# Performance work log

Hardware: AMD Instinct MI355X
Metric: run time of the kernel (lower is better)

Reference implementation:

```python
import jax, jax.numpy as jnp
import numpy as np

N, E, G = 10000, 160000, 64          # nodes, edges, graphs in batch
X_IN, HID, EDIM, H = 128, 128, 32, 4  # feature dims, edge dim, heads
NEG_SLOPE = 0.2


def setup_inputs() -> dict:
    key = jax.random.key(0)
    ks = jax.random.split(key, 24)
    def p(k, shape):
        return jax.random.normal(k, shape, jnp.float32) * 0.1
    inp = {
        "x": jax.random.normal(ks[0], (N, X_IN), jnp.float32),
        "edge_index": jax.random.randint(ks[1], (2, E), 0, N),
        "edge_attr": jax.random.normal(ks[2], (E, EDIM), jnp.float32),
        "batch": jnp.sort(jax.random.randint(ks[3], (N,), 0, G)),
    }
    dims = [(X_IN, HID), (HID, 2 * HID), (2 * HID, HID)]
    i = 4
    for l, (cin, cout) in enumerate(dims, 1):
        inp[f"W{l}"] = p(ks[i], (cin, H * cout)); i += 1   # node lin (bias-free, PyG default)
        inp[f"We{l}"] = p(ks[i], (EDIM, H * cout)); i += 1  # edge lin (bias=False in PyG)
        inp[f"as{l}"] = p(ks[i], (H, cout)); i += 1         # att_src
        inp[f"ad{l}"] = p(ks[i], (H, cout)); i += 1         # att_dst
        inp[f"ae{l}"] = p(ks[i], (H, cout)); i += 1         # att_edge
        inp[f"b{l}"] = jnp.zeros((cout,), jnp.float32); i += 1
    return inp


def _add_self_loops(src, dst, eattr, n):
    # PyG GATConv default: add_self_loops=True, fill_value='mean' ->
    # self-loop edge_attr = scatter-mean of incoming edge_attr per node.
    deg = jax.ops.segment_sum(jnp.ones_like(dst, jnp.float32), dst, num_segments=n)
    mean_e = jax.ops.segment_sum(eattr, dst, num_segments=n) / jnp.maximum(deg, 1.0)[:, None]
    loop = jnp.arange(n)
    return (jnp.concatenate([src, loop]), jnp.concatenate([dst, loop]),
            jnp.concatenate([eattr, mean_e], axis=0))


def _segment_softmax(logits, seg, n):
    # logits: [E2, H], softmax over edges grouped by destination node
    m = jax.ops.segment_max(logits, seg, num_segments=n)
    m = jnp.where(jnp.isfinite(m), m, 0.0)
    ex = jnp.exp(logits - m[seg])
    s = jax.ops.segment_sum(ex, seg, num_segments=n)
    return ex / (s[seg] + 1e-16)


def _gat_layer(x, src, dst, eattr, W, We, a_s, a_d, a_e, b, n):
    heads, cout = a_s.shape
    xs = (x @ W).reshape(n, heads, cout)            # [N,H,C]
    ee = (eattr @ We).reshape(-1, heads, cout)      # [E2,H,C]
    al_src = jnp.sum(xs * a_s, axis=-1)             # [N,H]
    al_dst = jnp.sum(xs * a_d, axis=-1)             # [N,H]
    al_edge = jnp.sum(ee * a_e, axis=-1)            # [E2,H]
    logits = jax.nn.leaky_relu(al_src[src] + al_dst[dst] + al_edge, NEG_SLOPE)
    alpha = _segment_softmax(logits, dst, n)        # [E2,H]
    out = jax.ops.segment_sum(alpha[:, :, None] * xs[src], dst, num_segments=n)
    return out.mean(axis=1) + b                     # concat=False -> mean over heads


def reference(x, edge_index, edge_attr, batch,
              W1, We1, as1, ad1, ae1, b1,
              W2, We2, as2, ad2, ae2, b2,
              W3, We3, as3, ad3, ae3, b3):
    src, dst = edge_index[0], edge_index[1]
    src2, dst2, e2 = _add_self_loops(src, dst, edge_attr, N)
    h = jax.nn.elu(_gat_layer(x, src2, dst2, e2, W1, We1, as1, ad1, ae1, b1, N))
    h = jax.nn.elu(_gat_layer(h, src2, dst2, e2, W2, We2, as2, ad2, ae2, b2, N))
    h = jax.nn.elu(_gat_layer(h, src2, dst2, e2, W3, We3, as3, ad3, ae3, b3, N))
    cnt = jax.ops.segment_sum(jnp.ones((N,), jnp.float32), batch, num_segments=G)
    return jax.ops.segment_sum(h, batch, num_segments=G) / jnp.maximum(cnt, 1.0)[:, None]
```

## Files before the change

kernel.cpp:

```cpp
#include <hip/hip_runtime.h>

#define NN 10000
#define NE 160000
#define NE2 (NE + NN)
#define NG 64
#define EDIM 32

typedef _Float16 f16;
typedef __attribute__((ext_vector_type(2))) _Float16 f16x2;
typedef __attribute__((ext_vector_type(4))) _Float16 f16x4;
typedef __attribute__((ext_vector_type(8))) _Float16 f16x8;
typedef __attribute__((ext_vector_type(4))) float f32x4;
typedef __attribute__((ext_vector_type(8))) unsigned short u16x8;

__device__ __forceinline__ float lrelu(float x) { return fmaxf(x, 0.2f * x); }
__device__ __forceinline__ float elu1(float x) { return x > 0.f ? x : __expf(x) - 1.f; }


template <int CIN, int C>
__device__ __forceinline__ void wprep_body(int b, int tid,
                                           const float* __restrict__ W,
                                           const float* __restrict__ We,
                                           const float* __restrict__ as_,
                                           const float* __restrict__ ad_,
                                           const float* __restrict__ ae_,
                                           f16* __restrict__ Bt,
                                           float* __restrict__ asd,
                                           float* __restrict__ Wf,
                                           float (*t)[33]) {
    constexpr int K4 = 4 * CIN;
    constexpr int KT = CIN / 32, CT = C / 32;
    constexpr int TB = 4 * KT * CT;
    constexpr int FB = CIN / 64;
    if (b < TB) {
        int h = b / (KT * CT);
        int rem = b % (KT * CT);
        int k0 = (rem / CT) * 32, c0 = (rem % CT) * 32;
        int i = tid >> 5, j = tid & 31;
#pragma unroll
        for (int it = 0; it < 4; ++it)
            t[i + it * 8][j] = W[(size_t)(k0 + i + it * 8) * (4 * C) + h * C + c0 + j];
        __syncthreads();
#pragma unroll
        for (int it = 0; it < 4; ++it) {
            int jj = (tid >> 5) + it * 8, ii = tid & 31;
            Bt[(size_t)(c0 + jj) * K4 + h * CIN + k0 + ii] = (f16)t[ii][jj];
        }
    } else if (b < TB + FB) {
        int k = (b - TB) * 64 + (tid >> 2), h = tid & 3;
        const float4* wr = (const float4*)(W + (size_t)k * (4 * C) + h * C);
        const float4* a4 = (const float4*)(as_ + h * C);
        const float4* d4 = (const float4*)(ad_ + h * C);
        float s = 0.f, d = 0.f;
        for (int c = 0; c < C / 4; ++c) {
            float4 w = wr[c], av = a4[c], dv = d4[c];
            s += w.x * av.x + w.y * av.y + w.z * av.z + w.w * av.w;
            d += w.x * dv.x + w.y * dv.y + w.z * dv.z + w.w * dv.w;
        }
        asd[h * CIN + k] = s;
        asd[4 * CIN + h * CIN + k] = d;
    } else if (tid < 128) {
        int dd = tid >> 2, h = tid & 3;
        const float4* wr = (const float4*)(We + (size_t)dd * (4 * C) + h * C);
        const float4* a4 = (const float4*)(ae_ + h * C);
        float s = 0.f;
        for (int c = 0; c < C / 4; ++c) {
            float4 w = wr[c], av = a4[c];
            s += w.x * av.x + w.y * av.y + w.z * av.z + w.w * av.w;
        }
        Wf[dd * 4 + h] = s;
    }
}


__global__ __launch_bounds__(256) void k_init(
    const float* W1, const float* We1, const float* as1, const float* ad1, const float* ae1,
    f16* Bt1, float* asd1, float* Wf1,
    const float* W2, const float* We2, const float* as2, const float* ad2, const float* ae2,
    f16* Bt2, float* asd2, float* Wf2,
    const float* W3, const float* We3, const float* as3, const float* ad3, const float* ae3,
    f16* Bt3, float* asd3, float* Wf3,
    const int* ei, int* deg, const float* x, f16* x16,
    const int* batch, float* invc) {
    __shared__ float t[32][33];
    int b = blockIdx.x, tid = threadIdx.x;
    if (b < 67) {
        wprep_body<128, 128>(b, tid, W1, We1, as1, ad1, ae1, Bt1, asd1, Wf1, t);
    } else if (b < 198) {
        wprep_body<128, 256>(b - 67, tid, W2, We2, as2, ad2, ae2, Bt2, asd2, Wf2, t);
    } else if (b < 331) {
        wprep_body<256, 128>(b - 198, tid, W3, We3, as3, ad3, ae3, Bt3, asd3, Wf3, t);
    } else if (b < 956) {
        int e = (b - 331) * 256 + tid;
        atomicAdd(&deg[ei[NE + e]], 1);
    } else if (b < 2206) {
        int i = (b - 956) * 256 + tid;
        float4 v = ((const float4*)x)[i];
        f16x4 o;
        o[0] = (f16)v.x; o[1] = (f16)v.y; o[2] = (f16)v.z; o[3] = (f16)v.w;
        *(f16x4*)(x16 + i * 4) = o;
    } else if (tid < NG) {
        int g = tid;
        int lo = 0, hi = NN;
        while (lo < hi) { int mid = (lo + hi) >> 1; if (batch[mid] < g) lo = mid + 1; else hi = mid; }
        int start = lo;
        lo = start; hi = NN;
        while (lo < hi) { int mid = (lo + hi) >> 1; if (batch[mid] < g + 1) lo = mid + 1; else hi = mid; }
        invc[g] = 1.f / fmaxf((float)(lo - start), 1.f);
    }
}


__global__ __launch_bounds__(1024) void k_scan2(const int* __restrict__ deg,
                                                int* __restrict__ row_ptr,
                                                int* __restrict__ cursor) {
    int tid = threadIdx.x;
    int vals[10];
    int run = 0;
#pragma unroll
    for (int i = 0; i < 10; ++i) {
        int n = tid * 10 + i;
        int v = (n < NN) ? (deg[n] + 1) : 0;
        run += v;
        vals[i] = run;
    }
    int total = run;
    int lane = tid & 63, wid = tid >> 6;
    int sc = total;
#pragma unroll
    for (int off = 1; off < 64; off <<= 1) {
        int t = __shfl_up(sc, off);
        if (lane >= off) sc += t;
    }
    __shared__ int wsum[16];
    if (lane == 63) wsum[wid] = sc;
    __syncthreads();
    if (tid == 0) {
        int a = 0;
#pragma unroll
        for (int w = 0; w < 16; ++w) { int t = wsum[w]; wsum[w] = a; a += t; }
    }
    __syncthreads();
    int excl = sc - total + wsum[wid];
#pragma unroll
    for (int i = 0; i < 10; ++i) {
        int n = tid * 10 + i;
        if (n < NN) {
            int prev = i ? vals[i - 1] : 0;
            row_ptr[n + 1] = excl + vals[i];
            cursor[n] = excl + prev;
        }
    }
    if (tid == 0) row_ptr[0] = 0;
}


__global__ __launch_bounds__(256) void k_fill_e4(const int* __restrict__ ei,
                                                 int* __restrict__ cursor,
                                                 int* __restrict__ src_sorted,
                                                 int* __restrict__ selfpos,
                                                 const float* __restrict__ eattr,
                                                 const float* __restrict__ Wf1,
                                                 const float* __restrict__ Wf2,
                                                 const float* __restrict__ Wf3,
                                                 float* __restrict__ e4all,
                                                 const f16* __restrict__ x16,
                                                 const float* __restrict__ asd1,
                                                 float* __restrict__ als1,
                                                 float* __restrict__ ald1) {
    __shared__ float smem[1024];
    int b = blockIdx.x, tid = threadIdx.x;
    if (b < 665) {
        for (int i = tid; i < 384; i += 256)
            smem[i] = (i < 128) ? Wf1[i] : (i < 256) ? Wf2[i - 128] : Wf3[i - 256];
        __syncthreads();
        int e = b * 256 + tid;
        if (e >= NE2) return;
        if (e < NE) {
            int s = ei[e], d = ei[NE + e];
            int p = atomicAdd(&cursor[d], 1);
            src_sorted[p] = s;
            float4 v[8];
            const float4* er = (const float4*)(eattr + (size_t)e * EDIM);
#pragma unroll
            for (int i = 0; i < 8; ++i) v[i] = er[i];
#pragma unroll
            for (int l = 0; l < 3; ++l) {
                float a0 = 0.f, a1 = 0.f, a2 = 0.f, a3 = 0.f;
#pragma unroll
                for (int d4 = 0; d4 < 8; ++d4) {
                    const float* w = &smem[l * 128 + d4 * 16];
                    a0 += v[d4].x * w[0] + v[d4].y * w[4] + v[d4].z * w[8]  + v[d4].w * w[12];
                    a1 += v[d4].x * w[1] + v[d4].y * w[5] + v[d4].z * w[9]  + v[d4].w * w[13];
                    a2 += v[d4].x * w[2] + v[d4].y * w[6] + v[d4].z * w[10] + v[d4].w * w[14];
                    a3 += v[d4].x * w[3] + v[d4].y * w[7] + v[d4].z * w[11] + v[d4].w * w[15];
                }
                ((float4*)e4all)[(size_t)l * NE2 + p] = make_float4(a0, a1, a2, a3);
            }
        } else {
            int n = e - NE;
            int p = atomicAdd(&cursor[n], 1);
            src_sorted[p] = n;
            selfpos[n] = p;
        }
    } else {
        float* sA = smem;
        float* sD = smem + 512;
        for (int i = tid; i < 512; i += 256) { sA[i] = asd1[i]; sD[i] = asd1[512 + i]; }
        __syncthreads();
        int wid = tid >> 6, lane = tid & 63;
        int node = (b - 665) * 4 + wid;
        int h = lane >> 4, c16 = lane & 15;
        const f16* xr = x16 + (size_t)node * 128 + c16 * 8;
        f16x8 v = *(const f16x8*)xr;
        float s = 0.f, d = 0.f;
#pragma unroll
        for (int i = 0; i < 8; ++i) {
            float f = (float)v[i];
            s += f * sA[h * 128 + c16 * 8 + i];
            d += f * sD[h * 128 + c16 * 8 + i];
        }
#pragma unroll
        for (int off = 1; off < 16; off <<= 1) { s += __shfl_xor(s, off); d += __shfl_xor(d, off); }
        if (c16 == 0) { als1[node * 4 + h] = s; ald1[node * 4 + h] = d; }
    }
}


template <int CIN>
__global__ __launch_bounds__(256) void k_alnode2(const f16* __restrict__ xp,
                                                 const float* __restrict__ asd,
                                                 float* __restrict__ als,
                                                 float* __restrict__ ald) {
    __shared__ float sA[4 * CIN], sD[4 * CIN];
    for (int i = threadIdx.x; i < 4 * CIN; i += 256) { sA[i] = asd[i]; sD[i] = asd[4 * CIN + i]; }
    __syncthreads();
    int wid = threadIdx.x >> 6, lane = threadIdx.x & 63;
    int node = blockIdx.x * 4 + wid;
    int h = lane >> 4, c16 = lane & 15;
    constexpr int KC = CIN / 16;
    const f16* xr = xp + (size_t)node * CIN + c16 * KC;
    float s = 0.f, d = 0.f;
#pragma unroll
    for (int p = 0; p < KC / 8; ++p) {
        f16x8 v = *(const f16x8*)(xr + p * 8);
        const float* wa = &sA[h * CIN + c16 * KC + p * 8];
        const float* wd = &sD[h * CIN + c16 * KC + p * 8];
#pragma unroll
        for (int i = 0; i < 8; ++i) {
            float f = (float)v[i];
            s += f * wa[i];
            d += f * wd[i];
        }
    }
#pragma unroll
    for (int off = 1; off < 16; off <<= 1) { s += __shfl_xor(s, off); d += __shfl_xor(d, off); }
    if (c16 == 0) { als[node * 4 + h] = s; ald[node * 4 + h] = d; }
}


template <int CIN, int WPN>
__global__ __launch_bounds__(256) void k_agg2(const int* __restrict__ row_ptr,
                                              const int* __restrict__ src_sorted,
                                              const int* __restrict__ selfpos,
                                              const float* __restrict__ e4,
                                              const float* __restrict__ als,
                                              const float* __restrict__ ald,
                                              const f16* __restrict__ xp,
                                              f16* __restrict__ aggcat) {
    constexpr int CHUNK = CIN / WPN;
    constexpr int EPL = CHUNK / 64;
    constexpr int NPB = 4 / WPN;
    int wid = threadIdx.x >> 6, lane = threadIdx.x & 63;
    int node = blockIdx.x * NPB + wid / WPN;
    int half = wid % WPN;
    int beg = row_ptr[node], end = row_ptr[node + 1];
    int sp = selfpos[node];
    float4 ad4 = ((const float4*)ald)[node];
    const float4* e44 = (const float4*)e4;
    const float4* als4 = (const float4*)als;
    float s0 = 0.f, s1 = 0.f, s2 = 0.f, s3 = 0.f;
    float es0 = 0.f, es1 = 0.f, es2 = 0.f, es3 = 0.f;
    float a0[EPL] = {}, a1[EPL] = {}, a2[EPL] = {}, a3[EPL] = {};
    const f16* xbase = xp + half * CHUNK + lane * EPL;
#pragma unroll 4
    for (int j = beg; j < end; ++j) {
        if (j == sp) continue;
        int src = src_sorted[j];
        float4 ev = e44[j];
        es0 += ev.x; es1 += ev.y; es2 += ev.z; es3 += ev.w;
        float4 av = als4[src];
        float e0 = __expf(lrelu(ev.x + av.x + ad4.x));
        float e1 = __expf(lrelu(ev.y + av.y + ad4.y));
        float e2 = __expf(lrelu(ev.z + av.z + ad4.z));
        float e3 = __expf(lrelu(ev.w + av.w + ad4.w));
        s0 += e0; s1 += e1; s2 += e2; s3 += e3;
        const f16* xr = xbase + (size_t)src * CIN;
        f16x2 v = *(const f16x2*)xr;
        float f0 = (float)v[0], f1 = (float)v[1];
        a0[0] += e0 * f0; a0[1] += e0 * f1;
        a1[0] += e1 * f0; a1[1] += e1 * f1;
        a2[0] += e2 * f0; a2[1] += e2 * f1;
        a3[0] += e3 * f0; a3[1] += e3 * f1;
    }
    {
        float inv = 1.f / fmaxf((float)(end - beg - 1), 1.f);
        float4 sv = als4[node];
        float e0 = __expf(lrelu(es0 * inv + sv.x + ad4.x));
        float e1 = __expf(lrelu(es1 * inv + sv.y + ad4.y));
        float e2 = __expf(lrelu(es2 * inv + sv.z + ad4.z));
        float e3 = __expf(lrelu(es3 * inv + sv.w + ad4.w));
        s0 += e0; s1 += e1; s2 += e2; s3 += e3;
        const f16* xr = xbase + (size_t)node * CIN;
        f16x2 v = *(const f16x2*)xr;
        float f0 = (float)v[0], f1 = (float)v[1];
        a0[0] += e0 * f0; a0[1] += e0 * f1;
        a1[0] += e1 * f0; a1[1] += e1 * f1;
        a2[0] += e2 * f0; a2[1] += e2 * f1;
        a3[0] += e3 * f0; a3[1] += e3 * f1;
    }
    float i0 = 1.f / (s0 + 1e-16f), i1 = 1.f / (s1 + 1e-16f);
    float i2 = 1.f / (s2 + 1e-16f), i3 = 1.f / (s3 + 1e-16f);
    f16* ob = aggcat + (size_t)node * 4 * CIN + half * CHUNK + lane * EPL;
    f16x2 o;
    o[0] = (f16)(a0[0] * i0); o[1] = (f16)(a0[1] * i0); *(f16x2*)(ob + 0 * CIN) = o;
    o[0] = (f16)(a1[0] * i1); o[1] = (f16)(a1[1] * i1); *(f16x2*)(ob + 1 * CIN) = o;
    o[0] = (f16)(a2[0] * i2); o[1] = (f16)(a2[1] * i2); *(f16x2*)(ob + 2 * CIN) = o;
    o[0] = (f16)(a3[0] * i3); o[1] = (f16)(a3[1] * i3); *(f16x2*)(ob + 3 * CIN) = o;
}


template <int K4, int C, bool POOL>
__global__ __launch_bounds__(256) void k_gemm2(const f16* __restrict__ A,
                                               const f16* __restrict__ Bt,
                                               const float* __restrict__ bias,
                                               f16* __restrict__ hout,
                                               const int* __restrict__ batch,
                                               const float* __restrict__ invc,
                                               float* __restrict__ out) {
    constexpr int NS = K4 / 32;
    __shared__ f16 Als[2][32 * 32];
    __shared__ f16 Bls[2][64 * 32];
    __shared__ float pacc[4][64];
    int bm = blockIdx.x * 32, bn = blockIdx.y * 64;
    int tid = threadIdx.x;
    int wid = tid >> 6, lane = tid & 63;
    int mq = wid >> 1, nq = wid & 1;
    int fr = lane & 15, kc = lane >> 4;

    if (POOL) pacc[tid >> 6][tid & 63] = 0.f;

    int ar = tid >> 2, ac = tid & 3;
    const f16* Ap = A + (size_t)(bm + (ar & 31)) * K4 + ac * 8;
    const f16* Bp = Bt + (size_t)(bn + ar) * K4 + ac * 8;
    bool aok = (tid < 128) && (bm + ar < NN);
    int wA = (ar & 31) * 32 + ((ac ^ (ar & 3)) * 8);
    int wB = ar * 32 + ((ac ^ (ar & 3)) * 8);
    int kx = (kc ^ (fr & 3)) * 8;
    int rA = (mq * 16 + fr) * 32 + kx;
    int rB0 = (nq * 32 + fr) * 32 + kx;
    int rB1 = rB0 + 16 * 32;

    f32x4 acc0 = (f32x4){0.f, 0.f, 0.f, 0.f};
    f32x4 acc1 = (f32x4){0.f, 0.f, 0.f, 0.f};

    u16x8 va = (u16x8)0, vb;
    if (aok) va = *(const u16x8*)Ap;
    vb = *(const u16x8*)Bp;
    if (tid < 128) *(u16x8*)&Als[0][wA] = va;
    *(u16x8*)&Bls[0][wB] = vb;
    __syncthreads();

#pragma unroll
    for (int s = 0; s < NS; ++s) {
        int cur = s & 1;
        if (s + 1 < NS) {
            va = (u16x8)0;
            if (aok) va = *(const u16x8*)(Ap + (s + 1) * 32);
            vb = *(const u16x8*)(Bp + (s + 1) * 32);
        }
        f16x8 af  = *(const f16x8*)&Als[cur][rA];
        f16x8 bf0 = *(const f16x8*)&Bls[cur][rB0];
        f16x8 bf1 = *(const f16x8*)&Bls[cur][rB1];
        acc0 = __builtin_amdgcn_mfma_f32_16x16x32_f16(af, bf0, acc0, 0, 0, 0);
        acc1 = __builtin_amdgcn_mfma_f32_16x16x32_f16(af, bf1, acc1, 0, 0, 0);
        if (s + 1 < NS) {
            if (tid < 128) *(u16x8*)&Als[cur ^ 1][wA] = va;
            *(u16x8*)&Bls[cur ^ 1][wB] = vb;
        }
        __syncthreads();
    }

    int cr = kc * 4, cc = fr;
    int lc0 = nq * 32 + cc, lc1 = lc0 + 16;
    int col0 = bn + lc0, col1 = bn + lc1;
    float b0 = bias[col0], b1 = bias[col1];
    int g0 = POOL ? batch[bm] : 0;
#pragma unroll
    for (int r = 0; r < 4; ++r) {
        int row = bm + mq * 16 + cr + r;
        if (row >= NN) continue;
        float v0 = elu1(0.25f * acc0[r] + b0);
        float v1 = elu1(0.25f * acc1[r] + b1);
        if (POOL) {
            int g = batch[row];
            float ic = invc[g];
            int wi = g - g0;
            if (wi < 4) {
                atomicAdd(&pacc[wi][lc0], v0 * ic);
                atomicAdd(&pacc[wi][lc1], v1 * ic);
            } else {
                atomicAdd(&out[(size_t)g * C + col0], v0 * ic);
                atomicAdd(&out[(size_t)g * C + col1], v1 * ic);
            }
        } else {
            f16* cp = hout + (size_t)row * C + col0;
            cp[0] = (f16)v0;
            cp[16] = (f16)v1;
        }
    }
    if (POOL) {
        __syncthreads();
        int wi = tid >> 6, c = tid & 63;
        float val = pacc[wi][c];
        int g = g0 + wi;
        if (val != 0.f && g < NG)
            atomicAdd(&out[(size_t)g * C + bn + c], val);
    }
}


struct Ws {
    f16 *x16, *hA, *hB, *aggcat, *Wt1, *Wt2, *Wt3;
    float *als1, *ald1, *als2, *ald2, *als3, *ald3;
    float *e4all, *asd1, *asd2, *asd3, *Wf1, *Wf2, *Wf3, *invc;
    int *deg, *row_ptr, *cursor, *src_sorted, *selfpos;
};

static void carve(void* base, Ws& w) {
    char* p = (char*)base;
    size_t off = 0;
    auto take = [&](size_t bytes) {
        off = (off + 255) & ~(size_t)255;
        void* r = p + off;
        off += bytes;
        return r;
    };
    w.x16        = (f16*)take((size_t)NN * 128 * 2);
    w.hA         = (f16*)take((size_t)NN * 128 * 2);
    w.hB         = (f16*)take((size_t)NN * 256 * 2);
    w.aggcat     = (f16*)take((size_t)NN * 1024 * 2);
    w.Wt1        = (f16*)take((size_t)512 * 128 * 2);
    w.Wt2        = (f16*)take((size_t)512 * 256 * 2);
    w.Wt3        = (f16*)take((size_t)1024 * 128 * 2);
    w.als1       = (float*)take((size_t)NN * 4 * 4);
    w.ald1       = (float*)take((size_t)NN * 4 * 4);
    w.als2       = (float*)take((size_t)NN * 4 * 4);
    w.ald2       = (float*)take((size_t)NN * 4 * 4);
    w.als3       = (float*)take((size_t)NN * 4 * 4);
    w.ald3       = (float*)take((size_t)NN * 4 * 4);
    w.e4all      = (float*)take((size_t)3 * NE2 * 4 * 4);
    w.asd1       = (float*)take(2 * 4 * 128 * 4);
    w.asd2       = (float*)take(2 * 4 * 128 * 4);
    w.asd3       = (float*)take(2 * 4 * 256 * 4);
    w.Wf1        = (float*)take(128 * 4);
    w.Wf2        = (float*)take(128 * 4);
    w.Wf3        = (float*)take(128 * 4);
    w.invc       = (float*)take(NG * 4);
    w.deg        = (int*)take((size_t)NN * 4);
    w.row_ptr    = (int*)take((size_t)(NN + 1) * 4);
    w.cursor     = (int*)take((size_t)NN * 4);
    w.src_sorted = (int*)take((size_t)NE2 * 4);
    w.selfpos    = (int*)take((size_t)NN * 4);
}

extern "C" void kernel_launch(void* const* d_in, const int* in_sizes, int n_in,
                              void* d_out, int out_size, void* d_ws, size_t ws_size,
                              hipStream_t stream) {
    const float* x     = (const float*)d_in[0];
    const int*   ei    = (const int*)d_in[1];
    const float* eattr = (const float*)d_in[2];
    const int*   batch = (const int*)d_in[3];
    const float* W[3]  = {(const float*)d_in[4],  (const float*)d_in[10], (const float*)d_in[16]};
    const float* We[3] = {(const float*)d_in[5],  (const float*)d_in[11], (const float*)d_in[17]};
    const float* as_[3]= {(const float*)d_in[6],  (const float*)d_in[12], (const float*)d_in[18]};
    const float* ad_[3]= {(const float*)d_in[7],  (const float*)d_in[13], (const float*)d_in[19]};
    const float* ae_[3]= {(const float*)d_in[8],  (const float*)d_in[14], (const float*)d_in[20]};
    const float* b_[3] = {(const float*)d_in[9],  (const float*)d_in[15], (const float*)d_in[21]};
    float* out = (float*)d_out;

    Ws w;
    carve(d_ws, w);

    hipMemsetAsync(w.deg, 0, (size_t)NN * 4, stream);
    hipMemsetAsync(out, 0, (size_t)NG * 128 * 4, stream);

    k_init<<<2207, 256, 0, stream>>>(
        W[0], We[0], as_[0], ad_[0], ae_[0], w.Wt1, w.asd1, w.Wf1,
        W[1], We[1], as_[1], ad_[1], ae_[1], w.Wt2, w.asd2, w.Wf2,
        W[2], We[2], as_[2], ad_[2], ae_[2], w.Wt3, w.asd3, w.Wf3,
        ei, w.deg, x, w.x16, batch, w.invc);

    k_scan2<<<1, 1024, 0, stream>>>(w.deg, w.row_ptr, w.cursor);

    k_fill_e4<<<3165, 256, 0, stream>>>(ei, w.cursor, w.src_sorted, w.selfpos, eattr,
                                        w.Wf1, w.Wf2, w.Wf3, w.e4all,
                                        w.x16, w.asd1, w.als1, w.ald1);

    const float* e4_1 = w.e4all;
    const float* e4_2 = w.e4all + (size_t)NE2 * 4;
    const float* e4_3 = w.e4all + (size_t)2 * NE2 * 4;

    k_agg2<128, 1><<<NN / 4, 256, 0, stream>>>(w.row_ptr, w.src_sorted, w.selfpos, e4_1,
                                               w.als1, w.ald1, w.x16, w.aggcat);
    k_gemm2<512, 128, false><<<dim3(313, 2), 256, 0, stream>>>(w.aggcat, w.Wt1, b_[0],
                                                               w.hA, nullptr, nullptr, nullptr);
    k_alnode2<128><<<NN / 4, 256, 0, stream>>>(w.hA, w.asd2, w.als2, w.ald2);
    k_agg2<128, 1><<<NN / 4, 256, 0, stream>>>(w.row_ptr, w.src_sorted, w.selfpos, e4_2,
                                               w.als2, w.ald2, w.hA, w.aggcat);
    k_gemm2<512, 256, false><<<dim3(313, 4), 256, 0, stream>>>(w.aggcat, w.Wt2, b_[1],
                                                               w.hB, nullptr, nullptr, nullptr);
    k_alnode2<256><<<NN / 4, 256, 0, stream>>>(w.hB, w.asd3, w.als3, w.ald3);
    k_agg2<256, 2><<<NN / 2, 256, 0, stream>>>(w.row_ptr, w.src_sorted, w.selfpos, e4_3,
                                               w.als3, w.ald3, w.hB, w.aggcat);
    k_gemm2<1024, 128, true><<<dim3(313, 2), 256, 0, stream>>>(w.aggcat, w.Wt3, b_[2],
                                                               nullptr, batch, w.invc, out);
}
```

Baseline: 316.6 us.

## Precompute per-edge attention exponentials and split aggregation edges across wave pairs

Adds a per-edge kernel that computes exp(leaky_relu(edge+src+dst logits)) into a buffer, using a new dst_sorted array, and a kernel that fills in each node's self-loop edge feature mean once up front. The aggregation kernel then reads these precomputed weights and splits each node's edges between two waves, combining their partial sums through shared memory. This takes the exp work and the self-loop special case out of the serial per-node loop and doubles wave parallelism per node. The cost is extra launches, an extra edge-sized buffer round trip through memory, and a block-wide sync in aggregation.

```diff
diff --git a/kernel.cpp b/kernel.cpp
--- a/kernel.cpp
+++ b/kernel.cpp
@@ -158,6 +158,7 @@
 __global__ __launch_bounds__(256) void k_fill_e4(const int* __restrict__ ei,
                                                  int* __restrict__ cursor,
                                                  int* __restrict__ src_sorted,
+                                                 int* __restrict__ dst_sorted,
                                                  int* __restrict__ selfpos,
                                                  const float* __restrict__ eattr,
                                                  const float* __restrict__ Wf1,
@@ -180,6 +181,7 @@
             int s = ei[e], d = ei[NE + e];
             int p = atomicAdd(&cursor[d], 1);
             src_sorted[p] = s;
+            dst_sorted[p] = d;
             float4 v[8];
             const float4* er = (const float4*)(eattr + (size_t)e * EDIM);
 #pragma unroll
@@ -201,6 +203,7 @@
             int n = e - NE;
             int p = atomicAdd(&cursor[n], 1);
             src_sorted[p] = n;
+            dst_sorted[p] = n;
             selfpos[n] = p;
         }
     } else {
@@ -224,6 +227,24 @@
         for (int off = 1; off < 16; off <<= 1) { s += __shfl_xor(s, off); d += __shfl_xor(d, off); }
         if (c16 == 0) { als1[node * 4 + h] = s; ald1[node * 4 + h] = d; }
     }
+}
+
+
+__global__ __launch_bounds__(256) void k_e4self(const int* __restrict__ row_ptr,
+                                                const int* __restrict__ selfpos,
+                                                float* __restrict__ e4all) {
+    int t = blockIdx.x * 256 + threadIdx.x;
+    int node = t >> 4, sub = t & 15;
+    if (sub >= 12) return;
+    int l = sub >> 2, c = sub & 3;
+    int beg = row_ptr[node], end = row_ptr[node + 1];
+    int sp = selfpos[node];
+    const float* base = e4all + (size_t)l * NE2 * 4 + c;
+    float s = 0.f;
+    for (int j = beg; j < end; ++j)
+        if (j != sp) s += base[(size_t)j * 4];
+    float inv = 1.f / fmaxf((float)(end - beg - 1), 1.f);
+    e4all[(size_t)l * NE2 * 4 + (size_t)sp * 4 + c] = s * inv;
 }
 
 
@@ -259,74 +280,83 @@
 }
 
 
-template <int CIN, int WPN>
-__global__ __launch_bounds__(256) void k_agg2(const int* __restrict__ row_ptr,
+__global__ __launch_bounds__(256) void k_t(const float* __restrict__ e4,
+                                           const int* __restrict__ src_sorted,
+                                           const int* __restrict__ dst_sorted,
+                                           const float* __restrict__ als,
+                                           const float* __restrict__ ald,
+                                           float* __restrict__ tbuf) {
+    int j = blockIdx.x * 256 + threadIdx.x;
+    if (j >= NE2) return;
+    float4 ev = ((const float4*)e4)[j];
+    int src = src_sorted[j], dst = dst_sorted[j];
+    float4 sv = ((const float4*)als)[src];
+    float4 dv = ((const float4*)ald)[dst];
+    float4 t;
+    t.x = __expf(lrelu(ev.x + sv.x + dv.x));
+    t.y = __expf(lrelu(ev.y + sv.y + dv.y));
+    t.z = __expf(lrelu(ev.z + sv.z + dv.z));
+    t.w = __expf(lrelu(ev.w + sv.w + dv.w));
+    ((float4*)tbuf)[j] = t;
+}
+
+
+template <int CIN, int CSPLIT>
+__global__ __launch_bounds__(256) void k_agg3(const int* __restrict__ row_ptr,
                                               const int* __restrict__ src_sorted,
-                                              const int* __restrict__ selfpos,
-                                              const float* __restrict__ e4,
-                                              const float* __restrict__ als,
-                                              const float* __restrict__ ald,
+                                              const float* __restrict__ tbuf,
                                               const f16* __restrict__ xp,
                                               f16* __restrict__ aggcat) {
-    constexpr int CHUNK = CIN / WPN;
+    constexpr int CHUNK = CIN / CSPLIT;
     constexpr int EPL = CHUNK / 64;
+    constexpr int WPN = 2 * CSPLIT;
     constexpr int NPB = 4 / WPN;
     int wid = threadIdx.x >> 6, lane = threadIdx.x & 63;
     int node = blockIdx.x * NPB + wid / WPN;
-    int half = wid % WPN;
+    int sub = wid % WPN;
+    int ch = sub >> 1;
+    int ep = sub & 1;
+    int pair = wid >> 1;
     int beg = row_ptr[node], end = row_ptr[node + 1];
-    int sp = selfpos[node];
-    float4 ad4 = ((const float4*)ald)[node];
-    const float4* e44 = (const float4*)e4;
-    const float4* als4 = (const float4*)als;
+    const float4* t4 = (const float4*)tbuf;
     float s0 = 0.f, s1 = 0.f, s2 = 0.f, s3 = 0.f;
-    float es0 = 0.f, es1 = 0.f, es2 = 0.f, es3 = 0.f;
     float a0[EPL] = {}, a1[EPL] = {}, a2[EPL] = {}, a3[EPL] = {};
-    const f16* xbase = xp + half * CHUNK + lane * EPL;
+    const f16* xbase = xp + ch * CHUNK + lane * EPL;
 #pragma unroll 4
-    for (int j = beg; j < end; ++j) {
-        if (j == sp) continue;
+    for (int j = beg + ep; j < end; j += 2) {
+        float4 t = t4[j];
         int src = src_sorted[j];
-        float4 ev = e44[j];
-        es0 += ev.x; es1 += ev.y; es2 += ev.z; es3 += ev.w;
-        float4 av = als4[src];
-        float e0 = __expf(lrelu(ev.x + av.x + ad4.x));
-        float e1 = __expf(lrelu(ev.y + av.y + ad4.y));
-        float e2 = __expf(lrelu(ev.z + av.z + ad4.z));
-        float e3 = __expf(lrelu(ev.w + av.w + ad4.w));
-        s0 += e0; s1 += e1; s2 += e2; s3 += e3;
-        const f16* xr = xbase + (size_t)src * CIN;
-        f16x2 v = *(const f16x2*)xr;
+        s0 += t.x; s1 += t.y; s2 += t.z; s3 += t.w;
+        f16x2 v = *(const f16x2*)(xbase + (size_t)src * CIN);
         float f0 = (float)v[0], f1 = (float)v[1];
-        a0[0] += e0 * f0; a0[1] += e0 * f1;
-        a1[0] += e1 * f0; a1[1] += e1 * f1;
-        a2[0] += e2 * f0; a2[1] += e2 * f1;
-        a3[0] += e3 * f0; a3[1] += e3 * f1;
-    }
-    {
-        float inv = 1.f / fmaxf((float)(end - beg - 1), 1.f);
-        float4 sv = als4[node];
-        float e0 = __expf(lrelu(es0 * inv + sv.x + ad4.x));
-        float e1 = __expf(lrelu(es1 * inv + sv.y + ad4.y));
-        float e2 = __expf(lrelu(es2 * inv + sv.z + ad4.z));
-        float e3 = __expf(lrelu(es3 * inv + sv.w + ad4.w));
-        s0 += e0; s1 += e1; s2 += e2; s3 += e3;
-        const f16* xr = xbase + (size_t)node * CIN;
-        f16x2 v = *(const f16x2*)xr;
-        float f0 = (float)v[0], f1 = (float)v[1];
-        a0[0] += e0 * f0; a0[1] += e0 * f1;
-        a1[0] += e1 * f0; a1[1] += e1 * f1;
-        a2[0] += e2 * f0; a2[1] += e2 * f1;
-        a3[0] += e3 * f0; a3[1] += e3 * f1;
-    }
-    float i0 = 1.f / (s0 + 1e-16f), i1 = 1.f / (s1 + 1e-16f);
-    float i2 = 1.f / (s2 + 1e-16f), i3 = 1.f / (s3 + 1e-16f);
-    f16* ob = aggcat + (size_t)node * 4 * CIN + half * CHUNK + lane * EPL;
-    f16x2 o;
-    o[0] = (f16)(a0[0] * i0); o[1] = (f16)(a0[1] * i0); *(f16x2*)(ob + 0 * CIN) = o;
-    o[0] = (f16)(a1[0] * i1); o[1] = (f16)(a1[1] * i1); *(f16x2*)(ob + 1 * CIN) = o;
-    o[0] = (f16)(a2[0] * i2); o[1] = (f16)(a2[1] * i2); *(f16x2*)(ob + 2 * CIN) = o;
-    o[0] = (f16)(a3[0] * i3); o[1] = (f16)(a3[1] * i3); *(f16x2*)(ob + 3 * CIN) = o;
+        a0[0] += t.x * f0; a0[1] += t.x * f1;
+        a1[0] += t.y * f0; a1[1] += t.y * f1;
+        a2[0] += t.z * f0; a2[1] += t.z * f1;
+        a3[0] += t.w * f0; a3[1] += t.w * f1;
+    }
+    __shared__ float lacc[2][64][8];
+    __shared__ float ls[2][4];
+    if (ep == 0) {
+        float* p = &lacc[pair][lane][0];
+        p[0] = a0[0]; p[1] = a0[1]; p[2] = a1[0]; p[3] = a1[1];
+        p[4] = a2[0]; p[5] = a2[1]; p[6] = a3[0]; p[7] = a3[1];
+        if (lane == 0) { ls[pair][0] = s0; ls[pair][1] = s1; ls[pair][2] = s2; ls[pair][3] = s3; }
+    }
+    __syncthreads();
+    if (ep == 1) {
+        const float* p = &lacc[pair][lane][0];
+        a0[0] += p[0]; a0[1] += p[1]; a1[0] += p[2]; a1[1] += p[3];
+        a2[0] += p[4]; a2[1] += p[5]; a3[0] += p[6]; a3[1] += p[7];
+        s0 += ls[pair][0]; s1 += ls[pair][1]; s2 += ls[pair][2]; s3 += ls[pair][3];
+        float i0 = 1.f / (s0 + 1e-16f), i1 = 1.f / (s1 + 1e-16f);
+        float i2 = 1.f / (s2 + 1e-16f), i3 = 1.f / (s3 + 1e-16f);
+        f16* ob = aggcat + (size_t)node * 4 * CIN + ch * CHUNK + lane * EPL;
+        f16x2 o;
+        o[0] = (f16)(a0[0] * i0); o[1] = (f16)(a0[1] * i0); *(f16x2*)(ob + 0 * CIN) = o;
+        o[0] = (f16)(a1[0] * i1); o[1] = (f16)(a1[1] * i1); *(f16x2*)(ob + 1 * CIN) = o;
+        o[0] = (f16)(a2[0] * i2); o[1] = (f16)(a2[1] * i2); *(f16x2*)(ob + 2 * CIN) = o;
+        o[0] = (f16)(a3[0] * i3); o[1] = (f16)(a3[1] * i3); *(f16x2*)(ob + 3 * CIN) = o;
+    }
 }
 
 
@@ -433,8 +463,8 @@
 struct Ws {
     f16 *x16, *hA, *hB, *aggcat, *Wt1, *Wt2, *Wt3;
     float *als1, *ald1, *als2, *ald2, *als3, *ald3;
-    float *e4all, *asd1, *asd2, *asd3, *Wf1, *Wf2, *Wf3, *invc;
-    int *deg, *row_ptr, *cursor, *src_sorted, *selfpos;
+    float *e4all, *tbuf, *asd1, *asd2, *asd3, *Wf1, *Wf2, *Wf3, *invc;
+    int *deg, *row_ptr, *cursor, *src_sorted, *dst_sorted, *selfpos;
 };
 
 static void carve(void* base, Ws& w) {
@@ -460,6 +490,7 @@
     w.als3       = (float*)take((size_t)NN * 4 * 4);
     w.ald3       = (float*)take((size_t)NN * 4 * 4);
     w.e4all      = (float*)take((size_t)3 * NE2 * 4 * 4);
+    w.tbuf       = (float*)take((size_t)NE2 * 4 * 4);
     w.asd1       = (float*)take(2 * 4 * 128 * 4);
     w.asd2       = (float*)take(2 * 4 * 128 * 4);
     w.asd3       = (float*)take(2 * 4 * 256 * 4);
@@ -471,6 +502,7 @@
     w.row_ptr    = (int*)take((size_t)(NN + 1) * 4);
     w.cursor     = (int*)take((size_t)NN * 4);
     w.src_sorted = (int*)take((size_t)NE2 * 4);
+    w.dst_sorted = (int*)take((size_t)NE2 * 4);
     w.selfpos    = (int*)take((size_t)NN * 4);
 }
 
@@ -503,26 +535,30 @@
 
     k_scan2<<<1, 1024, 0, stream>>>(w.deg, w.row_ptr, w.cursor);
 
-    k_fill_e4<<<3165, 256, 0, stream>>>(ei, w.cursor, w.src_sorted, w.selfpos, eattr,
-                                        w.Wf1, w.Wf2, w.Wf3, w.e4all,
+    k_fill_e4<<<3165, 256, 0, stream>>>(ei, w.cursor, w.src_sorted, w.dst_sorted,
+                                        w.selfpos, eattr, w.Wf1, w.Wf2, w.Wf3, w.e4all,
                                         w.x16, w.asd1, w.als1, w.ald1);
+    k_e4self<<<625, 256, 0, stream>>>(w.row_ptr, w.selfpos, w.e4all);
 
     const float* e4_1 = w.e4all;
     const float* e4_2 = w.e4all + (size_t)NE2 * 4;
     const float* e4_3 = w.e4all + (size_t)2 * NE2 * 4;
 
-    k_agg2<128, 1><<<NN / 4, 256, 0, stream>>>(w.row_ptr, w.src_sorted, w.selfpos, e4_1,
-                                               w.als1, w.ald1, w.x16, w.aggcat);
+    k_t<<<665, 256, 0, stream>>>(e4_1, w.src_sorted, w.dst_sorted, w.als1, w.ald1, w.tbuf);
+    k_agg3<128, 1><<<NN / 2, 256, 0, stream>>>(w.row_ptr, w.src_sorted, w.tbuf,
+                                               w.x16, w.aggcat);
     k_gemm2<512, 128, false><<<dim3(313, 2), 256, 0, stream>>>(w.aggcat, w.Wt1, b_[0],
                                                                w.hA, nullptr, nullptr, nullptr);
     k_alnode2<128><<<NN / 4, 256, 0, stream>>>(w.hA, w.asd2, w.als2, w.ald2);
-    k_agg2<128, 1><<<NN / 4, 256, 0, stream>>>(w.row_ptr, w.src_sorted, w.selfpos, e4_2,
-                                               w.als2, w.ald2, w.hA, w.aggcat);
+    k_t<<<665, 256, 0, stream>>>(e4_2, w.src_sorted, w.dst_sorted, w.als2, w.ald2, w.tbuf);
+    k_agg3<128, 1><<<NN / 2, 256, 0, stream>>>(w.row_ptr, w.src_sorted, w.tbuf,
+                                               w.hA, w.aggcat);
     k_gemm2<512, 256, false><<<dim3(313, 4), 256, 0, stream>>>(w.aggcat, w.Wt2, b_[1],
                                                                w.hB, nullptr, nullptr, nullptr);
     k_alnode2<256><<<NN / 4, 256, 0, stream>>>(w.hB, w.asd3, w.als3, w.ald3);
-    k_agg2<256, 2><<<NN / 2, 256, 0, stream>>>(w.row_ptr, w.src_sorted, w.selfpos, e4_3,
-                                               w.als3, w.ald3, w.hB, w.aggcat);
+    k_t<<<665, 256, 0, stream>>>(e4_3, w.src_sorted, w.dst_sorted, w.als3, w.ald3, w.tbuf);
+    k_agg3<256, 2><<<NN, 256, 0, stream>>>(w.row_ptr, w.src_sorted, w.tbuf,
+                                           w.hB, w.aggcat);
     k_gemm2<1024, 128, true><<<dim3(313, 2), 256, 0, stream>>>(w.aggcat, w.Wt3, b_[2],
                                                                nullptr, batch, w.invc, out);
 }
```

New measurement: 288.3 us. -8.9%, faster.

## Precompute edge attention weights in shared memory and split edges across two waves

Applied to the files above, without the earlier changes.

The aggregation kernel now has the whole block compute each edge's exp-logit once into shared memory, including the self-loop mean edge term via shared atomics, instead of every wave recomputing it. Each node's edge list is then split between two waves that process alternating edges and combine their partial sums through shared memory. This doubles wave-level parallelism per node and cuts redundant exp work and redundant per-edge loads. The cost is extra barriers, shared atomics, and a slow fallback path for nodes with more than 128 edges.

```diff
diff --git a/kernel.cpp b/kernel.cpp
--- a/kernel.cpp
+++ b/kernel.cpp
@@ -259,8 +259,8 @@
 }
 
 
-template <int CIN, int WPN>
-__global__ __launch_bounds__(256) void k_agg2(const int* __restrict__ row_ptr,
+template <int CIN, int CSPLIT>
+__global__ __launch_bounds__(256) void k_agg4(const int* __restrict__ row_ptr,
                                               const int* __restrict__ src_sorted,
                                               const int* __restrict__ selfpos,
                                               const float* __restrict__ e4,
@@ -268,65 +268,164 @@
                                               const float* __restrict__ ald,
                                               const f16* __restrict__ xp,
                                               f16* __restrict__ aggcat) {
-    constexpr int CHUNK = CIN / WPN;
+    constexpr int CHUNK = CIN / CSPLIT;
     constexpr int EPL = CHUNK / 64;
+    constexpr int WPN = 2 * CSPLIT;
     constexpr int NPB = 4 / WPN;
-    int wid = threadIdx.x >> 6, lane = threadIdx.x & 63;
-    int node = blockIdx.x * NPB + wid / WPN;
-    int half = wid % WPN;
+    constexpr int CAP = 128;
+
+    __shared__ float te4[NPB * CAP * 4];
+    __shared__ float lacc[2][64][8];
+    __shared__ float ls[2][4];
+    __shared__ float s4[NPB][4];
+    __shared__ int ovf;
+
+    int tid = threadIdx.x;
+    int wid = tid >> 6, lane = tid & 63;
+    int node0 = blockIdx.x * NPB;
+
+    if (tid < NPB * 4) s4[tid >> 2][tid & 3] = 0.f;
+    if (tid == 0) ovf = 0;
+    __syncthreads();
+
+    int tn = (NPB == 2) ? (tid >> 7) : 0;
+    int ts = (NPB == 2) ? (tid & 127) : tid;
+    int tnode = node0 + tn;
+    int tbeg = row_ptr[tnode];
+    int tcnt = row_ptr[tnode + 1] - tbeg;
+    int tsp = selfpos[tnode];
+    if (ts == 0 && tcnt > CAP) ovf = 1;
+    if (ts < CAP && ts < tcnt) {
+        int j = tbeg + ts;
+        float4 ev = ((const float4*)e4)[j];
+        ((float4*)te4)[tn * CAP + ts] = ev;
+        if (j != tsp) {
+            atomicAdd(&s4[tn][0], ev.x);
+            atomicAdd(&s4[tn][1], ev.y);
+            atomicAdd(&s4[tn][2], ev.z);
+            atomicAdd(&s4[tn][3], ev.w);
+        }
+    }
+    __syncthreads();
+
+    if (!ovf && ts < CAP && ts < tcnt) {
+        int j = tbeg + ts;
+        float4 ev = ((float4*)te4)[tn * CAP + ts];
+        float4 sv;
+        if (j == tsp) {
+            float inv = 1.f / fmaxf((float)(tcnt - 1), 1.f);
+            ev.x = s4[tn][0] * inv; ev.y = s4[tn][1] * inv;
+            ev.z = s4[tn][2] * inv; ev.w = s4[tn][3] * inv;
+            sv = ((const float4*)als)[tnode];
+        } else {
+            sv = ((const float4*)als)[src_sorted[j]];
+        }
+        float4 dv = ((const float4*)ald)[tnode];
+        float4 t;
+        t.x = __expf(lrelu(ev.x + sv.x + dv.x));
+        t.y = __expf(lrelu(ev.y + sv.y + dv.y));
+        t.z = __expf(lrelu(ev.z + sv.z + dv.z));
+        t.w = __expf(lrelu(ev.w + sv.w + dv.w));
+        ((float4*)te4)[tn * CAP + ts] = t;
+    }
+    __syncthreads();
+
+    int sub = wid % WPN;
+    int ch = sub >> 1, ep = sub & 1;
+    int pair = wid >> 1;
+    int node = node0 + wid / WPN;
     int beg = row_ptr[node], end = row_ptr[node + 1];
-    int sp = selfpos[node];
-    float4 ad4 = ((const float4*)ald)[node];
-    const float4* e44 = (const float4*)e4;
-    const float4* als4 = (const float4*)als;
+    const f16* xbase = xp + ch * CHUNK + lane * EPL;
+
+    if (ovf) {
+        if (ep == 1) return;
+        int sp = selfpos[node];
+        float4 ad4 = ((const float4*)ald)[node];
+        const float4* e44 = (const float4*)e4;
+        const float4* als4 = (const float4*)als;
+        float s0 = 0.f, s1 = 0.f, s2 = 0.f, s3 = 0.f;
+        float es0 = 0.f, es1 = 0.f, es2 = 0.f, es3 = 0.f;
+        float a0[2] = {}, a1[2] = {}, a2[2] = {}, a3[2] = {};
+        for (int j = beg; j < end; ++j) {
+            if (j == sp) continue;
+            int src = src_sorted[j];
+            float4 ev = e44[j];
+            es0 += ev.x; es1 += ev.y; es2 += ev.z; es3 += ev.w;
+            float4 av = als4[src];
+            float e0 = __expf(lrelu(ev.x + av.x + ad4.x));
+            float e1 = __expf(lrelu(ev.y + av.y + ad4.y));
+            float e2 = __expf(lrelu(ev.z + av.z + ad4.z));
+            float e3 = __expf(lrelu(ev.w + av.w + ad4.w));
+            s0 += e0; s1 += e1; s2 += e2; s3 += e3;
+            f16x2 v = *(const f16x2*)(xbase + (size_t)src * CIN);
+            float f0 = (float)v[0], f1 = (float)v[1];
+            a0[0] += e0 * f0; a0[1] += e0 * f1;
+            a1[0] += e1 * f0; a1[1] += e1 * f1;
+            a2[0] += e2 * f0; a2[1] += e2 * f1;
+            a3[0] += e3 * f0; a3[1] += e3 * f1;
+        }
+        {
+            float inv = 1.f / fmaxf((float)(end - beg - 1), 1.f);
+            float4 sv = ((const float4*)als)[node];
+            float e0 = __expf(lrelu(es0 * inv + sv.x + ad4.x));
+            float e1 = __expf(lrelu(es1 * inv + sv.y + ad4.y));
+            float e2 = __expf(lrelu(es2 * inv + sv.z + ad4.z));
+            float e3 = __expf(lrelu(es3 * inv + sv.w + ad4.w));
+            s0 += e0; s1 += e1; s2 += e2; s3 += e3;
+            f16x2 v = *(const f16x2*)(xbase + (size_t)node * CIN);
+            float f0 = (float)v[0], f1 = (float)v[1];
+            a0[0] += e0 * f0; a0[1] += e0 * f1;
+            a1[0] += e1 * f0; a1[1] += e1 * f1;
+            a2[0] += e2 * f0; a2[1] += e2 * f1;
+            a3[0] += e3 * f0; a3[1] += e3 * f1;
+        }
+        float i0 = 1.f / (s0 + 1e-16f), i1 = 1.f / (s1 + 1e-16f);
+        float i2 = 1.f / (s2 + 1e-16f), i3 = 1.f / (s3 + 1e-16f);
+        f16* ob = aggcat + (size_t)node * 4 * CIN + ch * CHUNK + lane * EPL;
+        f16x2 o;
+        o[0] = (f16)(a0[0] * i0); o[1] = (f16)(a0[1] * i0); *(f16x2*)(ob + 0 * CIN) = o;
+        o[0] = (f16)(a1[0] * i1); o[1] = (f16)(a1[1] * i1); *(f16x2*)(ob + 1 * CIN) = o;
+        o[0] = (f16)(a2[0] * i2); o[1] = (f16)(a2[1] * i2); *(f16x2*)(ob + 2 * CIN) = o;
+        o[0] = (f16)(a3[0] * i3); o[1] = (f16)(a3[1] * i3); *(f16x2*)(ob + 3 * CIN) = o;
+        return;
+    }
+
     float s0 = 0.f, s1 = 0.f, s2 = 0.f, s3 = 0.f;
-    float es0 = 0.f, es1 = 0.f, es2 = 0.f, es3 = 0.f;
-    float a0[EPL] = {}, a1[EPL] = {}, a2[EPL] = {}, a3[EPL] = {};
-    const f16* xbase = xp + half * CHUNK + lane * EPL;
+    float a0[2] = {}, a1[2] = {}, a2[2] = {}, a3[2] = {};
+    const float4* tt = (const float4*)te4 + (wid / WPN) * CAP;
 #pragma unroll 4
-    for (int j = beg; j < end; ++j) {
-        if (j == sp) continue;
+    for (int j = beg + ep; j < end; j += 2) {
+        float4 t = tt[j - beg];
         int src = src_sorted[j];
-        float4 ev = e44[j];
-        es0 += ev.x; es1 += ev.y; es2 += ev.z; es3 += ev.w;
-        float4 av = als4[src];
-        float e0 = __expf(lrelu(ev.x + av.x + ad4.x));
-        float e1 = __expf(lrelu(ev.y + av.y + ad4.y));
-        float e2 = __expf(lrelu(ev.z + av.z + ad4.z));
-        float e3 = __expf(lrelu(ev.w + av.w + ad4.w));
-        s0 += e0; s1 += e1; s2 += e2; s3 += e3;
-        const f16* xr = xbase + (size_t)src * CIN;
-        f16x2 v = *(const f16x2*)xr;
+        s0 += t.x; s1 += t.y; s2 += t.z; s3 += t.w;
+        f16x2 v = *(const f16x2*)(xbase + (size_t)src * CIN);
         float f0 = (float)v[0], f1 = (float)v[1];
-        a0[0] += e0 * f0; a0[1] += e0 * f1;
-        a1[0] += e1 * f0; a1[1] += e1 * f1;
-        a2[0] += e2 * f0; a2[1] += e2 * f1;
-        a3[0] += e3 * f0; a3[1] += e3 * f1;
-    }
-    {
-        float inv = 1.f / fmaxf((float)(end - beg - 1), 1.f);
-        float4 sv = als4[node];
-        float e0 = __expf(lrelu(es0 * inv + sv.x + ad4.x));
-        float e1 = __expf(lrelu(es1 * inv + sv.y + ad4.y));
-        float e2 = __expf(lrelu(es2 * inv + sv.z + ad4.z));
-        float e3 = __expf(lrelu(es3 * inv + sv.w + ad4.w));
-        s0 += e0; s1 += e1; s2 += e2; s3 += e3;
-        const f16* xr = xbase + (size_t)node * CIN;
-        f16x2 v = *(const f16x2*)xr;
-        float f0 = (float)v[0], f1 = (float)v[1];
-        a0[0] += e0 * f0; a0[1] += e0 * f1;
-        a1[0] += e1 * f0; a1[1] += e1 * f1;
-        a2[0] += e2 * f0; a2[1] += e2 * f1;
-        a3[0] += e3 * f0; a3[1] += e3 * f1;
-    }
-    float i0 = 1.f / (s0 + 1e-16f), i1 = 1.f / (s1 + 1e-16f);
-    float i2 = 1.f / (s2 + 1e-16f), i3 = 1.f / (s3 + 1e-16f);
-    f16* ob = aggcat + (size_t)node * 4 * CIN + half * CHUNK + lane * EPL;
-    f16x2 o;
-    o[0] = (f16)(a0[0] * i0); o[1] = (f16)(a0[1] * i0); *(f16x2*)(ob + 0 * CIN) = o;
-    o[0] = (f16)(a1[0] * i1); o[1] = (f16)(a1[1] * i1); *(f16x2*)(ob + 1 * CIN) = o;
-    o[0] = (f16)(a2[0] * i2); o[1] = (f16)(a2[1] * i2); *(f16x2*)(ob + 2 * CIN) = o;
-    o[0] = (f16)(a3[0] * i3); o[1] = (f16)(a3[1] * i3); *(f16x2*)(ob + 3 * CIN) = o;
+        a0[0] += t.x * f0; a0[1] += t.x * f1;
+        a1[0] += t.y * f0; a1[1] += t.y * f1;
+        a2[0] += t.z * f0; a2[1] += t.z * f1;
+        a3[0] += t.w * f0; a3[1] += t.w * f1;
+    }
+    if (ep == 0) {
+        float* p = &lacc[pair][lane][0];
+        p[0] = a0[0]; p[1] = a0[1]; p[2] = a1[0]; p[3] = a1[1];
+        p[4] = a2[0]; p[5] = a2[1]; p[6] = a3[0]; p[7] = a3[1];
+        if (lane == 0) { ls[pair][0] = s0; ls[pair][1] = s1; ls[pair][2] = s2; ls[pair][3] = s3; }
+    }
+    __syncthreads();
+    if (ep == 1) {
+        const float* p = &lacc[pair][lane][0];
+        a0[0] += p[0]; a0[1] += p[1]; a1[0] += p[2]; a1[1] += p[3];
+        a2[0] += p[4]; a2[1] += p[5]; a3[0] += p[6]; a3[1] += p[7];
+        s0 += ls[pair][0]; s1 += ls[pair][1]; s2 += ls[pair][2]; s3 += ls[pair][3];
+        float i0 = 1.f / (s0 + 1e-16f), i1 = 1.f / (s1 + 1e-16f);
+        float i2 = 1.f / (s2 + 1e-16f), i3 = 1.f / (s3 + 1e-16f);
+        f16* ob = aggcat + (size_t)node * 4 * CIN + ch * CHUNK + lane * EPL;
+        f16x2 o;
+        o[0] = (f16)(a0[0] * i0); o[1] = (f16)(a0[1] * i0); *(f16x2*)(ob + 0 * CIN) = o;
+        o[0] = (f16)(a1[0] * i1); o[1] = (f16)(a1[1] * i1); *(f16x2*)(ob + 1 * CIN) = o;
+        o[0] = (f16)(a2[0] * i2); o[1] = (f16)(a2[1] * i2); *(f16x2*)(ob + 2 * CIN) = o;
+        o[0] = (f16)(a3[0] * i3); o[1] = (f16)(a3[1] * i3); *(f16x2*)(ob + 3 * CIN) = o;
+    }
 }
 
 
@@ -511,18 +610,18 @@
     const float* e4_2 = w.e4all + (size_t)NE2 * 4;
     const float* e4_3 = w.e4all + (size_t)2 * NE2 * 4;
 
-    k_agg2<128, 1><<<NN / 4, 256, 0, stream>>>(w.row_ptr, w.src_sorted, w.selfpos, e4_1,
+    k_agg4<128, 1><<<NN / 2, 256, 0, stream>>>(w.row_ptr, w.src_sorted, w.selfpos, e4_1,
                                                w.als1, w.ald1, w.x16, w.aggcat);
     k_gemm2<512, 128, false><<<dim3(313, 2), 256, 0, stream>>>(w.aggcat, w.Wt1, b_[0],
                                                                w.hA, nullptr, nullptr, nullptr);
     k_alnode2<128><<<NN / 4, 256, 0, stream>>>(w.hA, w.asd2, w.als2, w.ald2);
-    k_agg2<128, 1><<<NN / 4, 256, 0, stream>>>(w.row_ptr, w.src_sorted, w.selfpos, e4_2,
+    k_agg4<128, 1><<<NN / 2, 256, 0, stream>>>(w.row_ptr, w.src_sorted, w.selfpos, e4_2,
                                                w.als2, w.ald2, w.hA, w.aggcat);
     k_gemm2<512, 256, false><<<dim3(313, 4), 256, 0, stream>>>(w.aggcat, w.Wt2, b_[1],
                                                                w.hB, nullptr, nullptr, nullptr);
     k_alnode2<256><<<NN / 4, 256, 0, stream>>>(w.hB, w.asd3, w.als3, w.ald3);
-    k_agg2<256, 2><<<NN / 2, 256, 0, stream>>>(w.row_ptr, w.src_sorted, w.selfpos, e4_3,
-                                               w.als3, w.ald3, w.hB, w.aggcat);
+    k_agg4<256, 2><<<NN, 256, 0, stream>>>(w.row_ptr, w.src_sorted, w.selfpos, e4_3,
+                                           w.als3, w.ald3, w.hB, w.aggcat);
     k_gemm2<1024, 128, true><<<dim3(313, 2), 256, 0, stream>>>(w.aggcat, w.Wt3, b_[2],
                                                                nullptr, batch, w.invc, out);
 }
```

Result: faster. 295.3 us (-6.7%).
